# Performance work log

Hardware: AMD Instinct MI355X
Metric: run time of the kernel (lower is better)

Reference implementation:

```python
import jax, jax.numpy as jnp
import numpy as np

TEMPERATURE = 1.0

def _logic_layer(x, sel_a, sel_b, gate_logits, temp):
    # x: [B, in], sel_a/sel_b: [n, in], gate_logits: [n, 16]
    a = jax.nn.softmax(sel_a / temp, axis=-1)
    b = jax.nn.softmax(sel_b / temp, axis=-1)
    p = jnp.einsum('bi,ni->bn', x, a)  # first soft operand  [B, n]
    q = jnp.einsum('bi,ni->bn', x, b)  # second soft operand [B, n]
    pq = p * q
    one = jnp.ones_like(p)
    zero = jnp.zeros_like(p)
    # 16 two-input probabilistic logic gates (difflogic ordering)
    gates = jnp.stack([
        zero,               # FALSE
        pq,                 # AND
        p - pq,             # A AND NOT B
        p,                  # A
        q - pq,             # NOT A AND B
        q,                  # B
        p + q - 2 * pq,     # XOR
        p + q - pq,         # OR
        one - (p + q - pq), # NOR
        one - (p + q - 2 * pq),  # XNOR
        one - q,            # NOT B
        one - q + pq,       # A OR NOT B
        one - p,            # NOT A
        one - p + pq,       # NOT A OR B
        one - pq,           # NAND
        one,                # TRUE
    ], axis=-1)  # [B, n, 16]
    w = jax.nn.softmax(gate_logits / temp, axis=-1)  # [n, 16]
    return jnp.einsum('bng,ng->bn', gates, w)


def setup_inputs() -> dict:
    key = jax.random.key(0)
    ks = jax.random.split(key, 13)
    B = 1048576  # 1024x1024 CA grid, flattened cells
    inp = {'x': jax.random.uniform(ks[0], (B, 9), dtype=jnp.float32)}
    dims = [(8, 9), (4, 8), (2, 4), (1, 2)]
    i = 1
    for li, (n, d) in enumerate(dims, start=1):
        inp[f'sa{li}'] = jax.random.normal(ks[i], (n, d), dtype=jnp.float32); i += 1
        inp[f'sb{li}'] = jax.random.normal(ks[i], (n, d), dtype=jnp.float32); i += 1
        inp[f'g{li}'] = jax.random.normal(ks[i], (n, 16), dtype=jnp.float32); i += 1
    return inp


def reference(x, sa1, sb1, g1, sa2, sb2, g2, sa3, sb3, g3, sa4, sb4, g4):
    t = TEMPERATURE
    h = _logic_layer(x, sa1, sb1, g1, t)   # [B, 8]
    h = _logic_layer(h, sa2, sb2, g2, t)   # [B, 4]
    h = _logic_layer(h, sa3, sb3, g3, t)   # [B, 2]
    h = _logic_layer(h, sa4, sb4, g4, t)   # [B, 1]
    return h
```

## Files before the change

### kernel.cpp

```cpp
#include <hip/hip_runtime.h>
#include <math.h>


#define THREADS 256
#define SPT 4
#define B_PER_BLOCK (THREADS * SPT)

template <int D>
__device__ __forceinline__ void softmax_row(const float* __restrict__ src,
                                            float* __restrict__ dst) {
    float e[D];
    float m = src[0];
    #pragma unroll
    for (int i = 1; i < D; ++i) m = fmaxf(m, src[i]);
    float s = 0.f;
    #pragma unroll
    for (int i = 0; i < D; ++i) { e[i] = __expf(src[i] - m); s += e[i]; }
    float inv = 1.f / s;
    #pragma unroll
    for (int i = 0; i < D; ++i) dst[i] = e[i] * inv;
}

__device__ __forceinline__ void gate_fold(const float* __restrict__ g,
                                          float* __restrict__ C) {
    const float k0[16]  = {0,0,0,0, 0,0,0,0, 1, 1, 1, 1, 1, 1, 1, 1};
    const float kp[16]  = {0,0,1,1, 0,0,1,1,-1,-1, 0, 0,-1,-1, 0, 0};
    const float kq[16]  = {0,0,0,0, 1,1,1,1,-1,-1,-1,-1, 0, 0, 0, 0};
    const float kpq[16] = {0,1,-1,0,-1,0,-2,-1, 1, 2, 0, 1, 0, 1,-1, 0};
    float w[16];
    float m = g[0];
    #pragma unroll
    for (int i = 1; i < 16; ++i) m = fmaxf(m, g[i]);
    float s = 0.f;
    #pragma unroll
    for (int i = 0; i < 16; ++i) { w[i] = __expf(g[i] - m); s += w[i]; }
    float inv = 1.f / s;
    float c0 = 0, c1 = 0, c2 = 0, c3 = 0;
    #pragma unroll
    for (int i = 0; i < 16; ++i) {
        float wi = w[i] * inv;
        c0 = fmaf(wi, k0[i], c0); c1 = fmaf(wi, kp[i], c1);
        c2 = fmaf(wi, kq[i], c2); c3 = fmaf(wi, kpq[i], c3);
    }
    C[0] = c0; C[1] = c1; C[2] = c2; C[3] = c3;
}

__global__ void coeff_kernel(const float* __restrict__ sa1, const float* __restrict__ sb1, const float* __restrict__ g1,
                             const float* __restrict__ sa2, const float* __restrict__ sb2, const float* __restrict__ g2,
                             const float* __restrict__ sa3, const float* __restrict__ sb3, const float* __restrict__ g3,
                             const float* __restrict__ sa4, const float* __restrict__ sb4, const float* __restrict__ g4,
                             float* __restrict__ cf) {
    const int t = threadIdx.x;
    if (t < 15) {
        int r = t;
        if      (r < 8)  softmax_row<9>(sa1 + r * 9,        cf + r * 9);
        else if (r < 12) softmax_row<8>(sa2 + (r - 8) * 8,  cf + 176 + (r - 8) * 8);
        else if (r < 14) softmax_row<4>(sa3 + (r - 12) * 4, cf + 256 + (r - 12) * 4);
        else             softmax_row<2>(sa4,                cf + 280);
    } else if (t >= 16 && t < 31) {
        int r = t - 16;
        if      (r < 8)  softmax_row<9>(sb1 + r * 9,        cf + 72 + r * 9);
        else if (r < 12) softmax_row<8>(sb2 + (r - 8) * 8,  cf + 208 + (r - 8) * 8);
        else if (r < 14) softmax_row<4>(sb3 + (r - 12) * 4, cf + 264 + (r - 12) * 4);
        else             softmax_row<2>(sb4,                cf + 282);
    } else if (t >= 32 && t < 47) {
        int r = t - 32;
        if      (r < 8)  gate_fold(g1 + r * 16,        cf + 144 + r * 4);
        else if (r < 12) gate_fold(g2 + (r - 8) * 16,  cf + 240 + (r - 8) * 4);
        else if (r < 14) gate_fold(g3 + (r - 12) * 16, cf + 272 + (r - 12) * 4);
        else             gate_fold(g4,                 cf + 284);
    }
}

__global__ __launch_bounds__(THREADS, 4) void net_kernel(
        const float* __restrict__ x, const float* __restrict__ cf,
        float* __restrict__ out, int nB) {
    const int T  = blockIdx.x * THREADS + threadIdx.x;
    const int b0 = T * SPT;
    if (b0 >= nB) return;

    float v[SPT][9];
    if (b0 + SPT <= nB) {
        const float4* __restrict__ x4 = (const float4*)x;
        float4 r[9];
        #pragma unroll
        for (int k = 0; k < 9; ++k) r[k] = x4[(long)T * 9 + k];
        const float* rf = (const float*)r;
        #pragma unroll
        for (int s = 0; s < SPT; ++s)
            #pragma unroll
            for (int i = 0; i < 9; ++i) v[s][i] = rf[s * 9 + i];
    } else {
        #pragma unroll
        for (int s = 0; s < SPT; ++s)
            #pragma unroll
            for (int i = 0; i < 9; ++i) {
                int b = b0 + s;
                v[s][i] = (b < nB) ? x[(long)b * 9 + i] : 0.f;
            }
    }

    float h1[SPT][8];
    #pragma unroll
    for (int j = 0; j < 8; ++j) {
        #pragma unroll
        for (int s = 0; s < SPT; ++s) {
            float p = 0.f, q = 0.f;
            #pragma unroll
            for (int i = 0; i < 9; ++i) {
                p = fmaf(v[s][i], cf[     j * 9 + i], p);
                q = fmaf(v[s][i], cf[72 + j * 9 + i], q);
            }
            h1[s][j] = fmaf(cf[144 + j*4 + 3], p * q,
                       fmaf(cf[144 + j*4 + 2], q,
                       fmaf(cf[144 + j*4 + 1], p, cf[144 + j*4 + 0])));
        }
    }
    float h2[SPT][4];
    #pragma unroll
    for (int j = 0; j < 4; ++j) {
        #pragma unroll
        for (int s = 0; s < SPT; ++s) {
            float p = 0.f, q = 0.f;
            #pragma unroll
            for (int i = 0; i < 8; ++i) {
                p = fmaf(h1[s][i], cf[176 + j * 8 + i], p);
                q = fmaf(h1[s][i], cf[208 + j * 8 + i], q);
            }
            h2[s][j] = fmaf(cf[240 + j*4 + 3], p * q,
                       fmaf(cf[240 + j*4 + 2], q,
                       fmaf(cf[240 + j*4 + 1], p, cf[240 + j*4 + 0])));
        }
    }
    float h3[SPT][2];
    #pragma unroll
    for (int j = 0; j < 2; ++j) {
        #pragma unroll
        for (int s = 0; s < SPT; ++s) {
            float p = 0.f, q = 0.f;
            #pragma unroll
            for (int i = 0; i < 4; ++i) {
                p = fmaf(h2[s][i], cf[256 + j * 4 + i], p);
                q = fmaf(h2[s][i], cf[264 + j * 4 + i], q);
            }
            h3[s][j] = fmaf(cf[272 + j*4 + 3], p * q,
                       fmaf(cf[272 + j*4 + 2], q,
                       fmaf(cf[272 + j*4 + 1], p, cf[272 + j*4 + 0])));
        }
    }
    float o[SPT];
    #pragma unroll
    for (int s = 0; s < SPT; ++s) {
        float p = fmaf(h3[s][0], cf[280], h3[s][1] * cf[281]);
        float q = fmaf(h3[s][0], cf[282], h3[s][1] * cf[283]);
        o[s] = fmaf(cf[287], p * q,
               fmaf(cf[286], q,
               fmaf(cf[285], p, cf[284])));
    }
    if (b0 + SPT <= nB) {
        float4* __restrict__ out4 = (float4*)out;
        float4 w; w.x = o[0]; w.y = o[1]; w.z = o[2]; w.w = o[3];
        out4[T] = w;
    } else {
        #pragma unroll
        for (int s = 0; s < SPT; ++s)
            if (b0 + s < nB) out[b0 + s] = o[s];
    }
}

extern "C" void kernel_launch(void* const* d_in, const int* in_sizes, int n_in,
                              void* d_out, int out_size, void* d_ws, size_t ws_size,
                              hipStream_t stream) {
    const float* x   = (const float*)d_in[0];
    const float* sa1 = (const float*)d_in[1];
    const float* sb1 = (const float*)d_in[2];
    const float* g1  = (const float*)d_in[3];
    const float* sa2 = (const float*)d_in[4];
    const float* sb2 = (const float*)d_in[5];
    const float* g2  = (const float*)d_in[6];
    const float* sa3 = (const float*)d_in[7];
    const float* sb3 = (const float*)d_in[8];
    const float* g3  = (const float*)d_in[9];
    const float* sa4 = (const float*)d_in[10];
    const float* sb4 = (const float*)d_in[11];
    const float* g4  = (const float*)d_in[12];
    float* cf = (float*)d_ws;
    const int nB = in_sizes[0] / 9;

    coeff_kernel<<<1, 64, 0, stream>>>(sa1, sb1, g1, sa2, sb2, g2,
                                       sa3, sb3, g3, sa4, sb4, g4, cf);
    const int grid = (nB + B_PER_BLOCK - 1) / B_PER_BLOCK;
    net_kernel<<<grid, THREADS, 0, stream>>>(x, cf, (float*)d_out, nB);
}
```

Before: 107.2 us.

## Stage input through shared memory with coalesced float4 loads, one sample per thread

```diff
diff --git a/kernel.cpp b/kernel.cpp
--- a/kernel.cpp
+++ b/kernel.cpp
@@ -3,8 +3,6 @@
 
 
 #define THREADS 256
-#define SPT 4
-#define B_PER_BLOCK (THREADS * SPT)
 
 template <int D>
 __device__ __forceinline__ void softmax_row(const float* __restrict__ src,
@@ -72,99 +70,83 @@
     }
 }
 
-__global__ __launch_bounds__(THREADS, 4) void net_kernel(
+__global__ __launch_bounds__(THREADS, 8) void net_kernel(
         const float* __restrict__ x, const float* __restrict__ cf,
         float* __restrict__ out, int nB) {
-    const int T  = blockIdx.x * THREADS + threadIdx.x;
-    const int b0 = T * SPT;
-    if (b0 >= nB) return;
+    __shared__ __align__(16) float xs[THREADS * 9];
 
-    float v[SPT][9];
-    if (b0 + SPT <= nB) {
-        const float4* __restrict__ x4 = (const float4*)x;
-        float4 r[9];
+    const int  tid   = threadIdx.x;
+    const long bBase = (long)blockIdx.x * THREADS;
+    const long fBase = bBase * 9;
+    const long totF  = (long)nB * 9;
+
+    {
+        int nF = (int)((totF - fBase < (long)(THREADS * 9)) ? (totF - fBase)
+                                                            : (THREADS * 9));
+        int n4 = nF >> 2;
+        const float4* __restrict__ x4 = (const float4*)(x + fBase);
         #pragma unroll
-        for (int k = 0; k < 9; ++k) r[k] = x4[(long)T * 9 + k];
-        const float* rf = (const float*)r;
-        #pragma unroll
-        for (int s = 0; s < SPT; ++s)
-            #pragma unroll
-            for (int i = 0; i < 9; ++i) v[s][i] = rf[s * 9 + i];
-    } else {
-        #pragma unroll
-        for (int s = 0; s < SPT; ++s)
-            #pragma unroll
-            for (int i = 0; i < 9; ++i) {
-                int b = b0 + s;
-                v[s][i] = (b < nB) ? x[(long)b * 9 + i] : 0.f;
-            }
+        for (int k = 0; k < 3; ++k) {
+            int idx = tid + k * THREADS;
+            if (idx < n4) *(float4*)(xs + idx * 4) = x4[idx];
+        }
+        for (int i = (n4 << 2) + tid; i < nF; i += THREADS)
+            xs[i] = x[fBase + i];
     }
+    __syncthreads();
 
-    float h1[SPT][8];
+    const long b = bBase + tid;
+    if (b >= nB) return;
+
+    float v[9];
+    #pragma unroll
+    for (int i = 0; i < 9; ++i) v[i] = xs[tid * 9 + i];
+
+    float h1[8];
     #pragma unroll
     for (int j = 0; j < 8; ++j) {
+        float p = 0.f, q = 0.f;
         #pragma unroll
-        for (int s = 0; s < SPT; ++s) {
-            float p = 0.f, q = 0.f;
-            #pragma unroll
-            for (int i = 0; i < 9; ++i) {
-                p = fmaf(v[s][i], cf[     j * 9 + i], p);
-                q = fmaf(v[s][i], cf[72 + j * 9 + i], q);
-            }
-            h1[s][j] = fmaf(cf[144 + j*4 + 3], p * q,
-                       fmaf(cf[144 + j*4 + 2], q,
-                       fmaf(cf[144 + j*4 + 1], p, cf[144 + j*4 + 0])));
+        for (int i = 0; i < 9; ++i) {
+            p = fmaf(v[i], cf[     j * 9 + i], p);
+            q = fmaf(v[i], cf[72 + j * 9 + i], q);
         }
+        h1[j] = fmaf(cf[144 + j*4 + 3], p * q,
+                fmaf(cf[144 + j*4 + 2], q,
+                fmaf(cf[144 + j*4 + 1], p, cf[144 + j*4 + 0])));
     }
-    float h2[SPT][4];
+    float h2[4];
     #pragma unroll
     for (int j = 0; j < 4; ++j) {
+        float p = 0.f, q = 0.f;
         #pragma unroll
-        for (int s = 0; s < SPT; ++s) {
-            float p = 0.f, q = 0.f;
-            #pragma unroll
-            for (int i = 0; i < 8; ++i) {
-                p = fmaf(h1[s][i], cf[176 + j * 8 + i], p);
-                q = fmaf(h1[s][i], cf[208 + j * 8 + i], q);
-            }
-            h2[s][j] = fmaf(cf[240 + j*4 + 3], p * q,
-                       fmaf(cf[240 + j*4 + 2], q,
-                       fmaf(cf[240 + j*4 + 1], p, cf[240 + j*4 + 0])));
+        for (int i = 0; i < 8; ++i) {
+            p = fmaf(h1[i], cf[176 + j * 8 + i], p);
+            q = fmaf(h1[i], cf[208 + j * 8 + i], q);
         }
+        h2[j] = fmaf(cf[240 + j*4 + 3], p * q,
+                fmaf(cf[240 + j*4 + 2], q,
+                fmaf(cf[240 + j*4 + 1], p, cf[240 + j*4 + 0])));
     }
-    float h3[SPT][2];
+    float h3[2];
     #pragma unroll
     for (int j = 0; j < 2; ++j) {
+        float p = 0.f, q = 0.f;
         #pragma unroll
-        for (int s = 0; s < SPT; ++s) {
-            float p = 0.f, q = 0.f;
-            #pragma unroll
-            for (int i = 0; i < 4; ++i) {
-                p = fmaf(h2[s][i], cf[256 + j * 4 + i], p);
-                q = fmaf(h2[s][i], cf[264 + j * 4 + i], q);
-            }
-            h3[s][j] = fmaf(cf[272 + j*4 + 3], p * q,
-                       fmaf(cf[272 + j*4 + 2], q,
-                       fmaf(cf[272 + j*4 + 1], p, cf[272 + j*4 + 0])));
+        for (int i = 0; i < 4; ++i) {
+            p = fmaf(h2[i], cf[256 + j * 4 + i], p);
+            q = fmaf(h2[i], cf[264 + j * 4 + i], q);
         }
+        h3[j] = fmaf(cf[272 + j*4 + 3], p * q,
+                fmaf(cf[272 + j*4 + 2], q,
+                fmaf(cf[272 + j*4 + 1], p, cf[272 + j*4 + 0])));
     }
-    float o[SPT];
-    #pragma unroll
-    for (int s = 0; s < SPT; ++s) {
-        float p = fmaf(h3[s][0], cf[280], h3[s][1] * cf[281]);
-        float q = fmaf(h3[s][0], cf[282], h3[s][1] * cf[283]);
-        o[s] = fmaf(cf[287], p * q,
-               fmaf(cf[286], q,
-               fmaf(cf[285], p, cf[284])));
-    }
-    if (b0 + SPT <= nB) {
-        float4* __restrict__ out4 = (float4*)out;
-        float4 w; w.x = o[0]; w.y = o[1]; w.z = o[2]; w.w = o[3];
-        out4[T] = w;
-    } else {
-        #pragma unroll
-        for (int s = 0; s < SPT; ++s)
-            if (b0 + s < nB) out[b0 + s] = o[s];
+    {
+        float p = fmaf(h3[0], cf[280], h3[1] * cf[281]);
+        float q = fmaf(h3[0], cf[282], h3[1] * cf[283]);
+        out[b] = fmaf(cf[287], p * q,
+                 fmaf(cf[286], q,
+                 fmaf(cf[285], p, cf[284])));
     }
 }
 
@@ -189,6 +171,6 @@
 
     coeff_kernel<<<1, 64, 0, stream>>>(sa1, sb1, g1, sa2, sb2, g2,
                                        sa3, sb3, g3, sa4, sb4, g4, cf);
-    const int grid = (nB + B_PER_BLOCK - 1) / B_PER_BLOCK;
+    const int grid = (nB + THREADS - 1) / THREADS;
     net_kernel<<<grid, THREADS, 0, stream>>>(x, cf, (float*)d_out, nB);
 }
```

Result: slower. 110.2 us (+2.8%).
